# Optimization experiments

Measured on AMD Instinct MI355X. Metric: run time of the kernel, lower is better.

## Reference

```python
import jax, jax.numpy as jnp
import numpy as np

B = 64
SIZES = [5023, 1256, 314, 79, 20]
NV = [s + 1 for s in SIZES]          # vertex counts incl. padding vertex
K = 12                               # spiral length (all levels)
LAT = 128
ENC_F = [3, 16, 32, 64, 128]
DEC_IN = [128, 64, 32, 32, 16]
DEC_OUT = [64, 32, 32, 16, 3]


def setup_inputs() -> dict:
    keys = iter(jax.random.split(jax.random.key(0), 80))

    def nrm(shape, scale=1.0):
        return jax.random.normal(next(keys), shape, jnp.float32) * scale

    inp = {}
    inp['x_talking'] = nrm((B, NV[0], 3))
    inp['template'] = nrm((B, NV[0], 3))
    for i in range(4):
        inp['D%d' % i] = nrm((NV[i + 1], NV[i]), 1.0 / np.sqrt(NV[i]))
        inp['U%d' % i] = nrm((NV[i], NV[i + 1]), 1.0 / np.sqrt(NV[i + 1]))
    for i in range(4):
        fan = ENC_F[i] * K
        inp['enc_w%d' % i] = nrm((ENC_F[i + 1], fan), 1.0 / np.sqrt(fan))
        inp['enc_b%d' % i] = jnp.zeros((ENC_F[i + 1],), jnp.float32)
    inp['fc_enc_w'] = nrm((LAT, NV[4] * DEC_IN[0]), 1.0 / np.sqrt(NV[4] * DEC_IN[0]))
    inp['fc_enc_b'] = jnp.zeros((LAT,), jnp.float32)
    inp['fc_dec_w'] = nrm((NV[4] * DEC_IN[0], 2 * LAT), 1.0 / np.sqrt(2 * LAT))
    inp['fc_dec_b'] = jnp.zeros((NV[4] * DEC_IN[0],), jnp.float32)
    for i in range(5):
        fan = DEC_IN[i] * K
        inp['dec_w%d' % i] = nrm((DEC_OUT[i], fan), 1.0 / np.sqrt(fan))
        inp['dec_b%d' % i] = jnp.zeros((DEC_OUT[i],), jnp.float32)
    for i in range(4):
        inp['S%d' % i] = jax.random.randint(next(keys), (NV[i], K), 0, NV[i], jnp.int32)
    return inp


def _spiral_conv(x, S, W, b, act):
    # x: [B, N, F]; S: [N, K] spiral neighbor indices; W: [out, K*F] (torch Linear layout)
    Bv, Nv, F = x.shape
    g = x[:, S, :].reshape(Bv, Nv, K * F)            # spiral neighbor gather
    y = act(jnp.einsum('bnf,of->bno', g, W) + b)     # gather-GEMM + activation
    mask = jnp.ones((1, Nv, 1), y.dtype).at[0, -1, 0].set(0.0)  # zero out padding vertex
    return y * mask


def _forward(x_talking, template, D, U, enc, fc_enc_w, fc_enc_b, fc_dec_w, fc_dec_b, dec, S):
    elu = jax.nn.elu
    # encode_talking
    x = x_talking
    for i in range(4):
        x = _spiral_conv(x, S[i], enc[i][0], enc[i][1], elu)
        x = jnp.einsum('mn,bnf->bmf', D[i], x)       # downsample
    z = x.reshape(B, -1) @ fc_enc_w.T + fc_enc_b     # [B, latent]
    # decode(z, z)
    h = jnp.concatenate([z, z], axis=1) @ fc_dec_w.T + fc_dec_b
    x = h.reshape(B, NV[4], DEC_IN[0])
    for i in range(3):
        x = jnp.einsum('mn,bnf->bmf', U[3 - i], x)   # upsample
        x = _spiral_conv(x, S[3 - i], dec[i][0], dec[i][1], elu)
    x = jnp.einsum('mn,bnf->bmf', U[0], x)
    x = _spiral_conv(x, S[0], dec[3][0], dec[3][1], elu)
    x = _spiral_conv(x, S[0], dec[4][0], dec[4][1], lambda v: v)  # identity activation
    return x, x + template


def reference(x_talking, template, D0, D1, D2, D3, U0, U1, U2, U3,
              enc_w0, enc_b0, enc_w1, enc_b1, enc_w2, enc_b2, enc_w3, enc_b3,
              fc_enc_w, fc_enc_b, fc_dec_w, fc_dec_b,
              dec_w0, dec_b0, dec_w1, dec_b1, dec_w2, dec_b2, dec_w3, dec_b3, dec_w4, dec_b4,
              S0, S1, S2, S3):
    return _forward(
        x_talking, template,
        [D0, D1, D2, D3], [U0, U1, U2, U3],
        [(enc_w0, enc_b0), (enc_w1, enc_b1), (enc_w2, enc_b2), (enc_w3, enc_b3)],
        fc_enc_w, fc_enc_b, fc_dec_w, fc_dec_b,
        [(dec_w0, dec_b0), (dec_w1, dec_b1), (dec_w2, dec_b2), (dec_w3, dec_b3), (dec_w4, dec_b4)],
        [S0, S1, S2, S3])
```

## Files before the change

### kernel.cpp

```cpp
#include <hip/hip_runtime.h>
#include <cstddef>


#define BATCH 64
#define SPK 12

typedef __attribute__((ext_vector_type(8))) short bf16x8;
typedef __attribute__((ext_vector_type(4))) short bf16x4;
typedef __attribute__((ext_vector_type(4))) float f32x4;

__device__ __forceinline__ unsigned short f2bf(float x) {
    union { float f; unsigned int u; } v; v.f = x;
    unsigned int r = v.u + 0x7FFF + ((v.u >> 16) & 1);
    return (unsigned short)(r >> 16);
}

__global__ __launch_bounds__(256) void prep_weights_kernel(
    const float* __restrict__ enc_w0, const float* __restrict__ enc_w1,
    const float* __restrict__ enc_w2, const float* __restrict__ enc_w3,
    const float* __restrict__ dec_w0, const float* __restrict__ dec_w1,
    const float* __restrict__ dec_w2, const float* __restrict__ dec_w3,
    const float* __restrict__ dec_w4, const float* __restrict__ dec_b4,
    float* __restrict__ WpE0, unsigned short* __restrict__ Wb_e1,
    unsigned short* __restrict__ Wb_c2, unsigned short* __restrict__ Wb_e2,
    unsigned short* __restrict__ Wb_e3, unsigned short* __restrict__ Wb_c0,
    unsigned short* __restrict__ Wb_c1, unsigned short* __restrict__ Wfs_c3,
    unsigned short* __restrict__ Wfs_c4, float* __restrict__ BpC4)
{
    int i = blockIdx.x * 256 + threadIdx.x;
    if (i < 1024) {
        int o = i >> 6, kf = i & 63, k = kf >> 2, f = kf & 3;
        WpE0[i] = (f < 3 && k < 12) ? enc_w0[o * 36 + k * 3 + f] : 0.f;
        return;
    }
    i -= 1024;
    if (i < 6144)  { Wb_e1[i] = f2bf(enc_w1[i]); return; }
    i -= 6144;
    if (i < 12288) { Wb_c2[i] = f2bf(dec_w2[i]); return; }
    i -= 12288;
    if (i < 24576) { Wb_e2[i] = f2bf(enc_w2[i]); return; }
    i -= 24576;
    if (i < 98304) { Wb_e3[i] = f2bf(enc_w3[i]); return; }
    i -= 98304;
    if (i < 98304) { Wb_c0[i] = f2bf(dec_w0[i]); return; }
    i -= 98304;
    if (i < 24576) { Wb_c1[i] = f2bf(dec_w1[i]); return; }
    i -= 24576;
    if (i < 6144) {
        int j = i & 7, lane = (i >> 3) & 63, s = i >> 9;
        int l15 = lane & 15, quad = (lane >> 4) & 3;
        Wfs_c3[i] = f2bf(dec_w3[l15 * 384 + s * 32 + quad * 8 + j]);
        return;
    }
    i -= 6144;
    if (i < 3072) {
        int j = i & 7, lane = (i >> 3) & 63, s = i >> 9;
        int l15 = lane & 15, quad = (lane >> 4) & 3;
        Wfs_c4[i] = (l15 < 3) ? f2bf(dec_w4[l15 * 192 + s * 32 + quad * 8 + j])
                              : (unsigned short)0;
        return;
    }
    i -= 3072;
    if (i < 16) BpC4[i] = (i < 3) ? dec_b4[i] : 0.f;
}
#define PREP_TOTAL (1024 + 6144 + 12288 + 24576 + 98304 + 98304 + 24576 + 6144 + 3072 + 16)

__global__ __launch_bounds__(256) void reducep_bf16_kernel(
    const float* __restrict__ P, size_t ps, unsigned short* __restrict__ out,
    int n8, int nparts)
{
    int i = blockIdx.x * 256 + threadIdx.x;
    if (i < n8) {
        size_t base = (size_t)i * 8;
        bf16x8 r;
#pragma unroll
        for (int j = 0; j < 8; ++j) {
            float v = __builtin_nontemporal_load(&P[base + j]);
            for (int p = 1; p < nparts; ++p)
                v += __builtin_nontemporal_load(&P[(size_t)p * ps + base + j]);
            r[j] = (short)f2bf(v);
        }
        *(bf16x8*)(out + base) = r;
    }
}

__global__ __launch_bounds__(256) void a_bf16_pad_kernel(
    const float* __restrict__ A, unsigned short* __restrict__ Ap,
    int M, int K, int Kp, int total)
{
    int i = blockIdx.x * 256 + threadIdx.x;
    if (i >= total) return;
    int kp8 = Kp >> 3;
    int m = i / kp8;
    int k0 = (i - m * kp8) * 8;
    bf16x8 r;
    if (m < M) {
        const float* src = A + (size_t)m * K + k0;
#pragma unroll
        for (int j = 0; j < 8; ++j) {
            float v = (k0 + j < K) ? src[j] : 0.f;
            r[j] = (short)f2bf(v);
        }
    } else {
#pragma unroll
        for (int j = 0; j < 8; ++j) r[j] = 0;
    }
    *(bf16x8*)(Ap + (size_t)m * Kp + k0) = r;
}

template<int LOGF, int OBF16>
__global__ __launch_bounds__(64, 4) void conv_cmfma_kernel(
    const unsigned short* __restrict__ x, const int* __restrict__ S,
    const unsigned short* __restrict__ Wfs, const float* __restrict__ bias,
    void* __restrict__ yv, int Nv, int elu_flag, int swz)
{
    constexpr int F     = 1 << LOGF;
    constexpr int KF    = SPK * F;
    constexpr int NS    = KF / 32;
    constexpr int RPADu = (LOGF == 5) ? 40 : 24;
    __shared__ unsigned short Gs[12 * 16 * RPADu];

    const int lane = threadIdx.x;
    const int l15  = lane & 15;
    const int quad = (lane >> 4) & 3;

    int bx = blockIdx.x, bz = blockIdx.z;
    if (swz) {
        const int gx = gridDim.x;
        const int total = gx * gridDim.z;
        int bid = bx + gx * bz;
        const int chunk = total >> 3;
        int sid = (bid & 7) * chunk + (bid >> 3);
        bx = sid % gx;
        bz = sid / gx;
    }
    const int n0 = bx * 16;
    const int b  = bz;
    const size_t xb = (size_t)b * Nv;

    int4 sv;
    {
        int g = lane >> 4; if (g > 2) g = 2;
        int n = n0 + l15; if (n >= Nv) n = 0;
        sv = *(const int4*)(S + n * SPK + g * 4);
    }

    if constexpr (LOGF == 5) {
        const int grow = lane >> 2, gchk = lane & 3;
#pragma unroll
        for (int k = 0; k < 12; ++k) {
            int sel = ((k >> 2) << 4) | grow;
            int comp = k & 3;
            int src = (comp == 0) ? __shfl(sv.x, sel)
                    : (comp == 1) ? __shfl(sv.y, sel)
                    : (comp == 2) ? __shfl(sv.z, sel)
                                  : __shfl(sv.w, sel);
            bf16x8 v = *(const bf16x8*)(x + ((xb + src) << 5) + gchk * 8);
            *(bf16x8*)&Gs[k * 16 * RPADu + grow * RPADu + gchk * 8] = v;
        }
    } else {
        const int khalf = lane >> 5, grow = (lane >> 1) & 15, gchk = lane & 1;
#pragma unroll
        for (int g = 0; g < 6; ++g) {
            int k0 = 2 * g;
            int sel0 = ((k0 >> 2) << 4) | grow;
            int sel1 = (((k0 + 1) >> 2) << 4) | grow;
            int s0 = ((k0 & 3) == 0) ? __shfl(sv.x, sel0) : __shfl(sv.z, sel0);
            int s1 = (((k0 + 1) & 3) == 1) ? __shfl(sv.y, sel1) : __shfl(sv.w, sel1);
            int src = khalf ? s1 : s0;
            int k   = k0 + khalf;
            bf16x8 v = *(const bf16x8*)(x + ((xb + src) << 4) + gchk * 8);
            *(bf16x8*)&Gs[k * 16 * RPADu + grow * RPADu + gchk * 8] = v;
        }
    }

    f32x4 acc0 = (f32x4){0.f, 0.f, 0.f, 0.f};
    f32x4 acc1 = (f32x4){0.f, 0.f, 0.f, 0.f};
#pragma unroll
    for (int s = 0; s < NS; ++s) {
        int kf = s * 32 + quad * 8;
        int k  = kf >> LOGF;
        int f  = kf & (F - 1);
        bf16x8 a = *(const bf16x8*)&Gs[k * 16 * RPADu + l15 * RPADu + f];
        bf16x8 w = *(const bf16x8*)(Wfs + (s * 64 + lane) * 8);
        if (s & 1) acc1 = __builtin_amdgcn_mfma_f32_16x16x32_bf16(a, w, acc1, 0, 0, 0);
        else       acc0 = __builtin_amdgcn_mfma_f32_16x16x32_bf16(a, w, acc0, 0, 0, 0);
    }

    float bv = bias[l15];
#pragma unroll
    for (int reg = 0; reg < 4; ++reg) {
        int nn = n0 + quad * 4 + reg;
        if (nn >= Nv) continue;
        float v = acc0[reg] + acc1[reg] + bv;
        if (elu_flag && v <= 0.f) v = expm1f(v);
        if (nn == Nv - 1) v = 0.f;
        size_t off = ((size_t)b * Nv + nn) * 16 + l15;
        if (OBF16) ((unsigned short*)yv)[off] = f2bf(v);
        else       ((float*)yv)[off] = v;
    }
}

template<int LOGF, int OBF16>
__global__ __launch_bounds__(64) void conv_wmfma_kernel(
    const unsigned short* __restrict__ x, const int* __restrict__ S,
    const unsigned short* __restrict__ Wb, const float* __restrict__ bias,
    void* __restrict__ yv, int Nv, int O, int elu_flag, int swz)
{
    constexpr int F  = 1 << LOGF;
    constexpr int KF = SPK * F;
    constexpr int NS = KF / 32;
    const int lane = threadIdx.x;
    const int l15  = lane & 15;
    const int quad = lane >> 4;

    int bx = blockIdx.x, by = blockIdx.y, bz = blockIdx.z;
    if (swz) {
        const int gx = gridDim.x, gy = gridDim.y;
        const int total = gx * gy * gridDim.z;
        int bid = bx + gx * (by + gy * bz);
        const int chunk = total >> 3;
        int sid = (bid & 7) * chunk + (bid >> 3);
        bx = sid % gx; sid /= gx;
        by = sid % gy;
        bz = sid / gy;
    }

    const int n0   = bx * 16;
    const int o    = by * 16 + l15;
    const int b    = bz;
    const size_t xb = (size_t)b * Nv;

    const int n  = n0 + l15;
    const int ng = (n < Nv) ? n : 0;
    const unsigned short* wrow = Wb + (size_t)o * KF;

    f32x4 acc0 = (f32x4){0.f, 0.f, 0.f, 0.f};
    f32x4 acc1 = (f32x4){0.f, 0.f, 0.f, 0.f};
#pragma unroll
    for (int s = 0; s < NS; ++s) {
        int kf  = s * 32 + quad * 8;
        int k   = kf >> LOGF;
        int f   = kf & (F - 1);
        int src = S[ng * SPK + k];
        bf16x8 a = *(const bf16x8*)(x + ((xb + src) << LOGF) + f);
        bf16x8 w = *(const bf16x8*)(wrow + kf);
        if (s & 1) acc1 = __builtin_amdgcn_mfma_f32_16x16x32_bf16(a, w, acc1, 0, 0, 0);
        else       acc0 = __builtin_amdgcn_mfma_f32_16x16x32_bf16(a, w, acc0, 0, 0, 0);
    }
    float bv = bias[o];
#pragma unroll
    for (int reg = 0; reg < 4; ++reg) {
        int nn = n0 + quad * 4 + reg;
        if (nn >= Nv) continue;
        float v = acc0[reg] + acc1[reg] + bv;
        if (elu_flag && v <= 0.f) v = expm1f(v);
        if (nn == Nv - 1) v = 0.f;
        size_t off = ((size_t)b * Nv + nn) * O + o;
        if (OBF16) ((unsigned short*)yv)[off] = f2bf(v);
        else       ((float*)yv)[off] = v;
    }
}

template<int LOGF>
__global__ __launch_bounds__(256) void conv_mfma32_kernel(
    const unsigned short* __restrict__ x, const int* __restrict__ S,
    const unsigned short* __restrict__ Wb, const float* __restrict__ bias,
    float* __restrict__ y, int Nv, int KF, int elu_flag)
{
    constexpr int PAD = 40;
    __shared__ unsigned short Gs[2][256 * PAD];

    const int b    = blockIdx.x;
    const int n0   = blockIdx.y * 256;
    const int tid  = threadIdx.x;
    const int lane = tid & 63;
    const int wave = tid >> 6;
    const int wm   = wave * 64;
    const int l15  = lane & 15;
    const int quad = lane >> 4;
    const size_t xb = (size_t)b * Nv;
    const int nslab = KF >> 5;

    f32x4 acc[4][2];
#pragma unroll
    for (int t = 0; t < 4; ++t)
#pragma unroll
        for (int o = 0; o < 2; ++o) acc[t][o] = (f32x4){0.f, 0.f, 0.f, 0.f};

    auto gath = [&](int k0, bf16x8* g) {
        int n = n0 + tid;
        if (n < Nv) {
#pragma unroll
            for (int j = 0; j < 4; ++j) {
                int kf  = k0 + j * 8;
                int k   = kf >> LOGF;
                int f   = kf & ((1 << LOGF) - 1);
                int src = S[n * SPK + k];
                g[j] = *(const bf16x8*)(x + ((xb + src) << LOGF) + f);
            }
        } else {
#pragma unroll
            for (int j = 0; j < 4; ++j)
#pragma unroll
                for (int e = 0; e < 8; ++e) g[j][e] = 0;
        }
    };
    auto put = [&](int buf, const bf16x8* g) {
#pragma unroll
        for (int j = 0; j < 4; ++j)
            *(bf16x8*)&Gs[buf][tid * PAD + j * 8] = g[j];
    };
    auto wfrag = [&](int k0, int o16) {
        return *(const bf16x8*)(Wb + (size_t)(o16 * 16 + l15) * KF + k0 + quad * 8);
    };

    bf16x8 gcur[4], gnext[4];
    gath(0, gcur);
    put(0, gcur);
    __syncthreads();

    for (int s = 0; s < nslab; ++s) {
        const int cur = s & 1;
        const bool more = (s + 1) < nslab;
        if (more) gath((s + 1) * 32, gnext);
        bf16x8 wf0 = wfrag(s * 32, 0);
        bf16x8 wf1 = wfrag(s * 32, 1);
#pragma unroll
        for (int t = 0; t < 4; ++t) {
            bf16x8 a = *(const bf16x8*)&Gs[cur][(wm + t * 16 + l15) * PAD + quad * 8];
            acc[t][0] = __builtin_amdgcn_mfma_f32_16x16x32_bf16(a, wf0, acc[t][0], 0, 0, 0);
            acc[t][1] = __builtin_amdgcn_mfma_f32_16x16x32_bf16(a, wf1, acc[t][1], 0, 0, 0);
        }
        if (more) {
            put(cur ^ 1, gnext);
            __syncthreads();
        }
    }

    float bv0 = bias[l15];
    float bv1 = bias[16 + l15];
#pragma unroll
    for (int t = 0; t < 4; ++t)
#pragma unroll
        for (int reg = 0; reg < 4; ++reg) {
            int n = n0 + wm + t * 16 + quad * 4 + reg;
            if (n >= Nv) continue;
            float v0 = acc[t][0][reg] + bv0;
            float v1 = acc[t][1][reg] + bv1;
            if (elu_flag) {
                if (v0 <= 0.f) v0 = expm1f(v0);
                if (v1 <= 0.f) v1 = expm1f(v1);
            }
            if (n == Nv - 1) { v0 = 0.f; v1 = 0.f; }
            size_t off = ((size_t)b * Nv + n) * 32 + l15;
            y[off]      = v0;
            y[off + 16] = v1;
        }
}

template<int OBF16, int NT>
__global__ __launch_bounds__(256) void dsamp_mfma3_kernel(
    const unsigned short* __restrict__ Ab, const unsigned short* __restrict__ Xt,
    void* __restrict__ Yv, int M, int Kp, int logF, int kchunk,
    int atomic_flag, int swz, size_t pstride)
{
    constexpr int PAD = 40;
    __shared__ unsigned short As[2][128 * PAD];
    __shared__ unsigned short Bs[2][128 * PAD];

    int bx = blockIdx.x, by = blockIdx.y, bz = blockIdx.z;
    if (swz) {
        const int gx = gridDim.x, gy = gridDim.y;
        const int total = gx * gy * gridDim.z;
        int bid = bx + gx * (by + gy * bz);
        const int chunk = total >> 3;
        int sid = (bid & 7) * chunk + (bid >> 3);
        bx = sid % gx; sid /= gx;
        by = sid % gy;
        bz = sid / gy;
    }

    const int fmask = (1 << logF) - 1;
    const int m0   = bx * 128;
    const int c0   = by * 128;
    const int kbeg = bz * kchunk;
    int kend = kbeg + kchunk; if (kend > Kp) kend = Kp;
    const int nslab = (kend - kbeg + 31) >> 5;
    const size_t zoff = (size_t)bz * pstride;

    const int tid  = threadIdx.x;
    const int lane = tid & 63;
    const int wave = tid >> 6;
    const int wm   = (wave >> 1) * 64;
    const int wn   = (wave & 1) * 64;
    const int l15  = lane & 15;
    const int quad = lane >> 4;

    const int s_row = tid >> 2;
    const int s_k8  = (tid & 3) * 8;

    f32x4 acc[4][4];
#pragma unroll
    for (int i = 0; i < 4; ++i)
#pragma unroll
        for (int j = 0; j < 4; ++j) acc[i][j] = (f32x4){0.f, 0.f, 0.f, 0.f};

    bf16x8 apre[2], bpre[2];

    auto loadAB = [&](int ko) {
        apre[0] = *(const bf16x8*)(Ab + (size_t)(m0 + s_row)      * Kp + ko + s_k8);
        apre[1] = *(const bf16x8*)(Ab + (size_t)(m0 + s_row + 64) * Kp + ko + s_k8);
        bpre[0] = *(const bf16x8*)(Xt + (size_t)(c0 + s_row)      * Kp + ko + s_k8);
        bpre[1] = *(const bf16x8*)(Xt + (size_t)(c0 + s_row + 64) * Kp + ko + s_k8);
    };
    auto stage = [&](int buf) {
        *(bf16x8*)&As[buf][s_row * PAD + s_k8]        = apre[0];
        *(bf16x8*)&As[buf][(s_row + 64) * PAD + s_k8] = apre[1];
        *(bf16x8*)&Bs[buf][s_row * PAD + s_k8]        = bpre[0];
        *(bf16x8*)&Bs[buf][(s_row + 64) * PAD + s_k8] = bpre[1];
    };

    loadAB(kbeg);
    stage(0);
    __syncthreads();

    for (int s = 0; s < nslab; ++s) {
        const int cur = s & 1;
        const bool more = (s + 1) < nslab;
        if (more) loadAB(kbeg + (s + 1) * 32);

        bf16x8 af[4], bfr[4];
#pragma unroll
        for (int t = 0; t < 4; ++t) {
            af[t]  = *(const bf16x8*)&As[cur][(wm + t * 16 + l15) * PAD + quad * 8];
            bfr[t] = *(const bf16x8*)&Bs[cur][(wn + t * 16 + l15) * PAD + quad * 8];
        }
#pragma unroll
        for (int tm = 0; tm < 4; ++tm)
#pragma unroll
            for (int tn = 0; tn < 4; ++tn)
                acc[tm][tn] = __builtin_amdgcn_mfma_f32_16x16x32_bf16(af[tm], bfr[tn], acc[tm][tn], 0, 0, 0);

        if (more) { stage(cur ^ 1); __syncthreads(); }
    }

#pragma unroll
    for (int tm = 0; tm < 4; ++tm)
#pragma unroll
        for (int tn = 0; tn < 4; ++tn)
#pragma unroll
            for (int reg = 0; reg < 4; ++reg) {
                int m  = m0 + wm + tm * 16 + quad * 4 + reg;
                int cc = c0 + wn + tn * 16 + l15;
                if (m < M) {
                    int bb = cc >> logF, f = cc & fmask;
                    size_t off = zoff + (((size_t)bb * M + m) << logF) + f;
                    float v = acc[tm][tn][reg];
                    if (OBF16)            ((unsigned short*)Yv)[off] = f2bf(v);
                    else if (atomic_flag) atomicAdd((float*)Yv + off, v);
                    else if (NT)          __builtin_nontemporal_store(v, (float*)Yv + off);
                    else                  ((float*)Yv)[off] = v;
                }
            }
}

template<int OBF16, int NT>
__global__ __launch_bounds__(256) void dsamp_mfma2_kernel(
    const unsigned short* __restrict__ Ap, const float* __restrict__ X,
    void* __restrict__ Yv, int M, int K, int Kp, int logF, int kchunk,
    int atomic_flag, size_t pstride)
{
    constexpr int PAD = 40;
    __shared__ unsigned short Xs[2][64 * PAD];

    const int fmask = (1 << logF) - 1;
    const int m0   = blockIdx.x * 64;
    const int c0   = blockIdx.y * 64;
    const int kbeg = blockIdx.z * kchunk;
    int kend = kbeg + kchunk; if (kend > K) kend = K;
    const int nslab = (kend - kbeg + 31) >> 5;
    const size_t zoff = (size_t)blockIdx.z * pstride;

    const int tid  = threadIdx.x;
    const int lane = tid & 63;
    const int wave = tid >> 6;
    const int wm   = (wave >> 1) * 32;
    const int wn   = (wave & 1) * 32;
    const int l15  = lane & 15;
    const int quad = lane >> 4;

    const int skk  = tid >> 4;
    const int scg  = (tid & 15) * 4;
    const int cB   = c0 + scg;
    const int xbb  = cB >> logF;
    const int xf   = cB & fmask;
    const size_t xrowbase = (((size_t)xbb * K) << logF) + xf;

    const int mA0 = m0 + wm + l15;
    const int mA1 = mA0 + 16;
    const int kaoff = quad * 8;

    f32x4 acc[2][2];
    acc[0][0] = acc[0][1] = acc[1][0] = acc[1][1] = (f32x4){0.f, 0.f, 0.f, 0.f};

    float4 xn0, xn1;
    bf16x8 ac0, ac1, an0, an1;

    {
        int k = kbeg + skk;
        xn0 = make_float4(0.f, 0.f, 0.f, 0.f);
        if (k < kend) xn0 = *(const float4*)(X + xrowbase + ((size_t)k << logF));
        k = kbeg + 16 + skk;
        xn1 = make_float4(0.f, 0.f, 0.f, 0.f);
        if (k < kend) xn1 = *(const float4*)(X + xrowbase + ((size_t)k << logF));
        int ka = kbeg + kaoff;
        ac0 = *(const bf16x8*)(Ap + (size_t)mA0 * Kp + ka);
        ac1 = *(const bf16x8*)(Ap + (size_t)mA1 * Kp + ka);
        unsigned short* p = &Xs[0][0];
        p[(scg + 0) * PAD + skk] = f2bf(xn0.x);
        p[(scg + 1) * PAD + skk] = f2bf(xn0.y);
        p[(scg + 2) * PAD + skk] = f2bf(xn0.z);
        p[(scg + 3) * PAD + skk] = f2bf(xn0.w);
        int kk1 = 16 + skk;
        p[(scg + 0) * PAD + kk1] = f2bf(xn1.x);
        p[(scg + 1) * PAD + kk1] = f2bf(xn1.y);
        p[(scg + 2) * PAD + kk1] = f2bf(xn1.z);
        p[(scg + 3) * PAD + kk1] = f2bf(xn1.w);
    }
    __syncthreads();

    for (int s = 0; s < nslab; ++s) {
        const int cur = s & 1;
        const bool more = (s + 1 < nslab);
        if (more) {
            int k0 = kbeg + (s + 1) * 32;
            int k = k0 + skk;
            xn0 = make_float4(0.f, 0.f, 0.f, 0.f);
            if (k < kend) xn0 = *(const float4*)(X + xrowbase + ((size_t)k << logF));
            k = k0 + 16 + skk;
            xn1 = make_float4(0.f, 0.f, 0.f, 0.f);
            if (k < kend) xn1 = *(const float4*)(X + xrowbase + ((size_t)k << logF));
            int ka = k0 + kaoff;
            an0 = *(const bf16x8*)(Ap + (size_t)mA0 * Kp + ka);
            an1 = *(const bf16x8*)(Ap + (size_t)mA1 * Kp + ka);
        }
        {
            const unsigned short* p = &Xs[cur][0];
            bf16x8 b0 = *(const bf16x8*)&p[(wn +      l15) * PAD + quad * 8];
            bf16x8 b1 = *(const bf16x8*)&p[(wn + 16 + l15) * PAD + quad * 8];
            acc[0][0] = __builtin_amdgcn_mfma_f32_16x16x32_bf16(ac0, b0, acc[0][0], 0, 0, 0);
            acc[0][1] = __builtin_amdgcn_mfma_f32_16x16x32_bf16(ac0, b1, acc[0][1], 0, 0, 0);
            acc[1][0] = __builtin_amdgcn_mfma_f32_16x16x32_bf16(ac1, b0, acc[1][0], 0, 0, 0);
            acc[1][1] = __builtin_amdgcn_mfma_f32_16x16x32_bf16(ac1, b1, acc[1][1], 0, 0, 0);
        }
        if (more) {
            unsigned short* q = &Xs[cur ^ 1][0];
            q[(scg + 0) * PAD + skk] = f2bf(xn0.x);
            q[(scg + 1) * PAD + skk] = f2bf(xn0.y);
            q[(scg + 2) * PAD + skk] = f2bf(xn0.z);
            q[(scg + 3) * PAD + skk] = f2bf(xn0.w);
            int kk1 = 16 + skk;
            q[(scg + 0) * PAD + kk1] = f2bf(xn1.x);
            q[(scg + 1) * PAD + kk1] = f2bf(xn1.y);
            q[(scg + 2) * PAD + kk1] = f2bf(xn1.z);
            q[(scg + 3) * PAD + kk1] = f2bf(xn1.w);
            __syncthreads();
            ac0 = an0; ac1 = an1;
        }
    }

#pragma unroll
    for (int tm = 0; tm < 2; ++tm)
#pragma unroll
        for (int tn = 0; tn < 2; ++tn)
#pragma unroll
            for (int reg = 0; reg < 4; ++reg) {
                int m  = m0 + wm + tm * 16 + quad * 4 + reg;
                int cc = c0 + wn + tn * 16 + l15;
                if (m < M) {
                    int bb = cc >> logF, f = cc & fmask;
                    size_t off = zoff + (((size_t)bb * M + m) << logF) + f;
                    float v = acc[tm][tn][reg];
                    if (OBF16)            ((unsigned short*)Yv)[off] = f2bf(v);
                    else if (atomic_flag) atomicAdd((float*)Yv + off, v);
                    else if (NT)          __builtin_nontemporal_store(v, (float*)Yv + off);
                    else                  ((float*)Yv)[off] = v;
                }
            }
}

template<int MT, int OT>
__global__ __launch_bounds__(256) void conv_gemm_kernel(
    const float* __restrict__ x, const int* __restrict__ S,
    const float* __restrict__ W, const float* __restrict__ bias,
    float* __restrict__ y, int Nv, int logF, int O, int KF, int KFr,
    int elu_flag)
{
    constexpr int CT = OT / 4;
    constexpr int RT = 256 / CT;
    static_assert(RT * 4 == MT, "tile shape");
    __shared__ float Gs[32][MT];
    __shared__ float Ws[32][OT];

    const int b   = blockIdx.x;
    const int n0  = blockIdx.y * MT;
    const int tid = threadIdx.x;
    const int cx  = tid % CT;
    const int ry  = tid / CT;
    const int r0  = ry * 4;
    const int o0  = cx * 4;
    const int fmask = (1 << logF) - 1;
    const size_t xb = (size_t)b * Nv;

    float acc[4][4];
#pragma unroll
    for (int i = 0; i < 4; ++i)
#pragma unroll
        for (int j = 0; j < 4; ++j) acc[i][j] = 0.f;

    for (int k0 = 0; k0 < KF; k0 += 32) {
        constexpr int GSLOTS = MT * 8;
#pragma unroll
        for (int i = 0; i < GSLOTS / 256; ++i) {
            int idx = tid + i * 256;
            int r   = idx & (MT - 1);
            int jg  = idx / MT;
            int j0  = jg * 4;
            int n   = n0 + r;
            int kf  = k0 + j0;
            float4 v = make_float4(0.f, 0.f, 0.f, 0.f);
            if (n < Nv && kf < KFr) {
                int k   = kf >> logF;
                int f   = kf & fmask;
                int src = S[n * SPK + k];
                v = *(const float4*)(x + ((xb + src) << logF) + f);
            }
            Gs[j0 + 0][r] = v.x; Gs[j0 + 1][r] = v.y;
            Gs[j0 + 2][r] = v.z; Gs[j0 + 3][r] = v.w;
        }
        constexpr int WSLOTS = OT * 8;
#pragma unroll
        for (int i = 0; i < (WSLOTS + 255) / 256; ++i) {
            int idx = tid + i * 256;
            if (WSLOTS >= 256 || idx < WSLOTS) {
                int o  = idx & (OT - 1);
                int jg = idx / OT;
                int j0 = jg * 4;
                float4 v = *(const float4*)(W + (size_t)o * KF + k0 + j0);
                Ws[j0 + 0][o] = v.x; Ws[j0 + 1][o] = v.y;
                Ws[j0 + 2][o] = v.z; Ws[j0 + 3][o] = v.w;
            }
        }
        __syncthreads();
#pragma unroll
        for (int kk = 0; kk < 32; ++kk) {
            float4 g = *(const float4*)&Gs[kk][r0];
            float4 w = *(const float4*)&Ws[kk][o0];
            acc[0][0] += g.x * w.x; acc[0][1] += g.x * w.y; acc[0][2] += g.x * w.z; acc[0][3] += g.x * w.w;
            acc[1][0] += g.y * w.x; acc[1][1] += g.y * w.y; acc[1][2] += g.y * w.z; acc[1][3] += g.y * w.w;
            acc[2][0] += g.z * w.x; acc[2][1] += g.z * w.y; acc[2][2] += g.z * w.z; acc[2][3] += g.z * w.w;
            acc[3][0] += g.w * w.x; acc[3][1] += g.w * w.y; acc[3][2] += g.w * w.z; acc[3][3] += g.w * w.w;
        }
        __syncthreads();
    }

    float4 bv = *(const float4*)(bias + o0);
#pragma unroll
    for (int i = 0; i < 4; ++i) {
        int n = n0 + r0 + i;
        if (n >= Nv) continue;
        float v0 = acc[i][0] + bv.x;
        float v1 = acc[i][1] + bv.y;
        float v2 = acc[i][2] + bv.z;
        float v3 = acc[i][3] + bv.w;
        if (elu_flag) {
            v0 = v0 > 0.f ? v0 : expm1f(v0);
            v1 = v1 > 0.f ? v1 : expm1f(v1);
            v2 = v2 > 0.f ? v2 : expm1f(v2);
            v3 = v3 > 0.f ? v3 : expm1f(v3);
        }
        if (n == Nv - 1) { v0 = v1 = v2 = v3 = 0.f; }
        *(float4*)(y + ((size_t)b * Nv + n) * O + o0) = make_float4(v0, v1, v2, v3);
    }
}

template<int OBF16>
__global__ __launch_bounds__(256) void dsamp_kernel(
    const float* __restrict__ A, const float* __restrict__ X,
    void* __restrict__ Yv, int M, int N, int F)
{
    __shared__ float As[16][68];
    __shared__ float Xs[16][64];

    const int m0  = blockIdx.x * 64;
    const int c0  = blockIdx.y * 64;
    const int tid = threadIdx.x;
    const int tx  = tid & 15;
    const int ty  = tid >> 4;

    float acc[4][4];
#pragma unroll
    for (int i = 0; i < 4; ++i)
#pragma unroll
        for (int j = 0; j < 4; ++j) acc[i][j] = 0.f;

    for (int k0 = 0; k0 < N; k0 += 16) {
#pragma unroll
        for (int p = 0; p < 4; ++p) {
            int r  = (tid >> 4) + p * 16;
            int kk = tid & 15;
            int m  = m0 + r;
            int n  = k0 + kk;
            float v = 0.f;
            if (m < M && n < N) v = A[(size_t)m * N + n];
            As[kk][r] = v;
        }
        {
            int kk = tid >> 4;
            int cc = (tid & 15) * 4;
            int n  = k0 + kk;
            float4 v = make_float4(0.f, 0.f, 0.f, 0.f);
            if (n < N) {
                int c  = c0 + cc;
                int bb = c / F;
                int f  = c - bb * F;
                v = *(const float4*)(X + ((size_t)bb * N + n) * F + f);
            }
            *(float4*)&Xs[kk][cc] = v;
        }
        __syncthreads();
#pragma unroll
        for (int kk = 0; kk < 16; ++kk) {
            float4 av = *(const float4*)&As[kk][ty * 4];
            float4 xv = *(const float4*)&Xs[kk][tx * 4];
            acc[0][0] += av.x * xv.x; acc[0][1] += av.x * xv.y; acc[0][2] += av.x * xv.z; acc[0][3] += av.x * xv.w;
            acc[1][0] += av.y * xv.x; acc[1][1] += av.y * xv.y; acc[1][2] += av.y * xv.z; acc[1][3] += av.y * xv.w;
            acc[2][0] += av.z * xv.x; acc[2][1] += av.z * xv.y; acc[2][2] += av.z * xv.z; acc[2][3] += av.z * xv.w;
            acc[3][0] += av.w * xv.x; acc[3][1] += av.w * xv.y; acc[3][2] += av.w * xv.z; acc[3][3] += av.w * xv.w;
        }
        __syncthreads();
    }

    const int cbase = c0 + tx * 4;
    const int bb = cbase / F;
    const int f  = cbase - bb * F;
#pragma unroll
    for (int i = 0; i < 4; ++i) {
        int m = m0 + ty * 4 + i;
        if (m < M) {
            size_t off = ((size_t)bb * M + m) * F + f;
            if (OBF16) {
                bf16x4 v;
                v[0] = (short)f2bf(acc[i][0]); v[1] = (short)f2bf(acc[i][1]);
                v[2] = (short)f2bf(acc[i][2]); v[3] = (short)f2bf(acc[i][3]);
                *(bf16x4*)((unsigned short*)Yv + off) = v;
            } else {
                *(float4*)((float*)Yv + off) =
                    make_float4(acc[i][0], acc[i][1], acc[i][2], acc[i][3]);
            }
        }
    }
}

__global__ __launch_bounds__(256) void fc_wave_kernel(
    const float* __restrict__ in, const float* __restrict__ W,
    const float* __restrict__ bias, float* __restrict__ out,
    int In, int O, int dup)
{
    const int gw   = blockIdx.x * 4 + (threadIdx.x >> 6);
    const int lane = threadIdx.x & 63;
    const int b = gw / O;
    const int o = gw - b * O;
    const float* xr = in + (size_t)b * In;
    float acc = 0.f;
    if (dup) {
        const float* wr = W + (size_t)o * (2 * In);
        for (int k = lane; k < In; k += 64)
            acc += xr[k] * (wr[k] + wr[In + k]);
    } else {
        const float* wr = W + (size_t)o * In;
        for (int k = lane; k < In; k += 64)
            acc += xr[k] * wr[k];
    }
#pragma unroll
    for (int off = 32; off > 0; off >>= 1)
        acc += __shfl_down(acc, off, 64);
    if (lane == 0) out[(size_t)b * O + o] = acc + bias[o];
}

__global__ __launch_bounds__(256) void xpose_bf16_kernel(
    const float* __restrict__ x, unsigned short* __restrict__ xt,
    int K, int Kp, int logF)
{
    const int c  = blockIdx.y * 256 + threadIdx.x;
    const int k0 = blockIdx.x * 8;
    const int bb = c >> logF;
    const int f  = c & ((1 << logF) - 1);
    const float* src = x + (((size_t)bb * K) << logF) + f;
    bf16x8 r;
#pragma unroll
    for (int j = 0; j < 8; ++j) {
        int k = k0 + j;
        float v = (k < K) ? src[(size_t)k << logF] : 0.f;
        r[j] = (short)f2bf(v);
    }
    *(bf16x8*)(xt + (size_t)c * Kp + k0) = r;
}

__global__ __launch_bounds__(256) void pad_x4_kernel(
    const float* __restrict__ x, float* __restrict__ xp, int n)
{
    int i = blockIdx.x * 256 + threadIdx.x;
    if (i < n) {
        int f = i & 3, nb = i >> 2;
        xp[i] = (f < 3) ? x[nb * 3 + f] : 0.f;
    }
}
__global__ __launch_bounds__(256) void extract_add_kernel(
    const float* __restrict__ cp, const float* __restrict__ t,
    float* __restrict__ o0, float* __restrict__ o1, int n)
{
    int i = blockIdx.x * 256 + threadIdx.x;
    if (i < n) {
        int f = i % 3, nb = i / 3;
        float v = cp[(size_t)nb * 16 + f];
        o0[i] = v;
        o1[i] = v + t[i];
    }
}


static inline int ilog2(int v) { int l = 0; while ((1 << l) < v) ++l; return l; }

static inline void a_bf16_launch(const float* A, unsigned short* Ap, int M, int K,
                                 int Mp, int Kp, hipStream_t s)
{
    int total = Mp * (Kp >> 3);
    a_bf16_pad_kernel<<<(total + 255) / 256, 256, 0, s>>>(A, Ap, M, K, Kp, total);
}

template<int OBF16, int NT>
static inline void dsamp_mfma2_launch(const unsigned short* Ap, const float* X,
                                      void* Y, int M, int K, int Kp, int F,
                                      int ks, int partial, hipStream_t s)
{
    int kchunk = (K + ks - 1) / ks;
    kchunk = (kchunk + 31) & ~31;
    int ksz = (K + kchunk - 1) / kchunk;
    int atomic = (ksz > 1 && !partial) ? 1 : 0;
    size_t pstride = (partial && ksz > 1) ? (size_t)BATCH * M * F : 0;
    dim3 grid((M + 63) / 64, F, ksz);
    dsamp_mfma2_kernel<OBF16, NT><<<grid, 256, 0, s>>>(Ap, X, Y, M, K, Kp, ilog2(F),
                                                       kchunk, atomic, pstride);
}

template<int OBF16, int NT>
static inline void dsamp_mfma3_launch(const unsigned short* Ab, const unsigned short* Xt,
                                      void* Y, int M, int Kp, int F,
                                      int ks, int partial, hipStream_t s)
{
    int slabs = Kp >> 5;
    int kchunk = ((slabs + ks - 1) / ks) * 32;
    int ksz = (Kp + kchunk - 1) / kchunk;
    int gx = (M + 127) / 128, gy = (BATCH * F) / 128;
    int total = gx * gy * ksz;
    int swz = ((total & 7) == 0) ? 1 : 0;
    int atomic = (ksz > 1 && !partial) ? 1 : 0;
    size_t pstride = (partial && ksz > 1) ? (size_t)BATCH * M * F : 0;
    dim3 grid(gx, gy, ksz);
    dsamp_mfma3_kernel<OBF16, NT><<<grid, 256, 0, s>>>(Ab, Xt, Y, M, Kp, ilog2(F),
                                                       kchunk, atomic, swz, pstride);
}

template<int OBF16>
static inline void dsamp_launch(const float* A, const float* X, void* Y,
                                int M, int N, int F, hipStream_t s)
{
    dim3 grid((M + 63) / 64, F);
    dsamp_kernel<OBF16><<<grid, 256, 0, s>>>(A, X, Y, M, N, F);
}

extern "C" void kernel_launch(void* const* d_in, const int* in_sizes, int n_in,
                              void* d_out, int out_size, void* d_ws, size_t ws_size,
                              hipStream_t stream)
{
    const float* x_talking = (const float*)d_in[0];
    const float* templ     = (const float*)d_in[1];
    const float* D0 = (const float*)d_in[2];
    const float* U0 = (const float*)d_in[3];
    const float* D1 = (const float*)d_in[4];
    const float* U1 = (const float*)d_in[5];
    const float* D2 = (const float*)d_in[6];
    const float* U2 = (const float*)d_in[7];
    const float* D3 = (const float*)d_in[8];
    const float* U3 = (const float*)d_in[9];
    const float* enc_w0 = (const float*)d_in[10]; const float* enc_b0 = (const float*)d_in[11];
    const float* enc_w1 = (const float*)d_in[12]; const float* enc_b1 = (const float*)d_in[13];
    const float* enc_w2 = (const float*)d_in[14]; const float* enc_b2 = (const float*)d_in[15];
    const float* enc_w3 = (const float*)d_in[16]; const float* enc_b3 = (const float*)d_in[17];
    const float* fc_enc_w = (const float*)d_in[18]; const float* fc_enc_b = (const float*)d_in[19];
    const float* fc_dec_w = (const float*)d_in[20]; const float* fc_dec_b = (const float*)d_in[21];
    const float* dec_w0 = (const float*)d_in[22]; const float* dec_b0 = (const float*)d_in[23];
    const float* dec_w1 = (const float*)d_in[24]; const float* dec_b1 = (const float*)d_in[25];
    const float* dec_w2 = (const float*)d_in[26]; const float* dec_b2 = (const float*)d_in[27];
    const float* dec_w3 = (const float*)d_in[28]; const float* dec_b3 = (const float*)d_in[29];
    const float* dec_w4 = (const float*)d_in[30]; const float* dec_b4 = (const float*)d_in[31];
    const int* S0 = (const int*)d_in[32];
    const int* S1 = (const int*)d_in[33];
    const int* S2 = (const int*)d_in[34];
    const int* S3 = (const int*)d_in[35];

    float* bufA = (float*)d_ws;
    float* bufB = bufA + 10289152;

    float* out0 = (float*)d_out;
    float* out1 = out0 + 964608;

    unsigned short* Xt_e0 = (unsigned short*)(bufB + 1290240);
    unsigned short* Xt_c2 = (unsigned short*)bufB;
    unsigned short* U0b   = (unsigned short*)(bufB + 1400000);
    unsigned short* Wb_e2 = (unsigned short*)(bufB + 4700000);
    unsigned short* Wb_e3 = (unsigned short*)(bufB + 4715000);
    unsigned short* Wb_c0 = (unsigned short*)(bufB + 4765000);
    unsigned short* Wb_c1 = (unsigned short*)(bufB + 4815000);
    unsigned short* D2b   = (unsigned short*)(bufB + 4830000);
    unsigned short* U2b   = (unsigned short*)(bufB + 4860000);
    float* xpad   = bufA + 5200000;
    unsigned short* D0b   = (unsigned short*)(bufA + 6700000);
    unsigned short* D1b   = (unsigned short*)(bufA + 9950000);
    unsigned short* U1b   = (unsigned short*)(bufA + 4000000);
    unsigned short* Wb_e1 = (unsigned short*)(bufA + 10160000);
    unsigned short* Wb_c2 = (unsigned short*)(bufA + 10170000);
    unsigned short* Wfs_c3 = (unsigned short*)(bufA + 10180000);
    unsigned short* Wfs_c4 = (unsigned short*)(bufA + 10185000);
    float* BpC4   = bufA + 10190000;
    float* WpE0   = bufA + 10195000;
    float*          Pd0   = bufA;
    unsigned short* Xb_e1 = (unsigned short*)bufB;
    float*          Pd1   = bufA + 5200000;
    unsigned short* Xb_e2   = (unsigned short*)(bufA + 2000000);
    float*          Pd2   = bufB;
    unsigned short* Xb_e3   = (unsigned short*)(bufA + 2000000);
    unsigned short* Xb_c2in = (unsigned short*)(bufA + 2600000);
    unsigned short* Xb_c3n  = (unsigned short*)bufA;
    unsigned short* Xb_c4   = (unsigned short*)(bufA + 5200000);

    prep_weights_kernel<<<(PREP_TOTAL + 255) / 256, 256, 0, stream>>>(
        enc_w0, enc_w1, enc_w2, enc_w3, dec_w0, dec_w1, dec_w2, dec_w3,
        dec_w4, dec_b4, WpE0, Wb_e1, Wb_c2, Wb_e2, Wb_e3, Wb_c0, Wb_c1,
        Wfs_c3, Wfs_c4, BpC4);
    pad_x4_kernel<<<5024, 256, 0, stream>>>(x_talking, xpad, 1286144);
    a_bf16_launch(D0, D0b, 1257, 5024, 1280, 5024, stream);
    a_bf16_launch(D1, D1b, 315, 1257, 320, 1280, stream);
    a_bf16_launch(D2, D2b, 80, 315, 128, 320, stream);
    a_bf16_launch(U2, U2b, 315, 80, 320, 96, stream);

    {
        dim3 grid(BATCH, (5024 + 255) / 256);
        conv_gemm_kernel<256, 16><<<grid, 256, 0, stream>>>(
            xpad, S0, WpE0, enc_b0, bufA, 5024, 2, 16, 64, 48, 1);
    }
    xpose_bf16_kernel<<<dim3(628, 4), 256, 0, stream>>>(bufA, Xt_e0, 5024, 5024, 4);
    dsamp_mfma3_launch<0, 1>(D0b, Xt_e0, Pd0, 1257, 5024, 16, 5, 1, stream);
    reducep_bf16_kernel<<<629, 256, 0, stream>>>(Pd0, 1287168, Xb_e1, 160896, 5);
    a_bf16_launch(U0, U0b, 5024, 1257, 5120, 1280, stream);
    a_bf16_launch(U1, U1b, 1257, 315, 1280, 320, stream);
    {
        dim3 grid(BATCH, (1257 + 255) / 256);
        conv_mfma32_kernel<4><<<grid, 256, 0, stream>>>(
            Xb_e1, S1, Wb_e1, enc_b1, bufA, 1257, 192, 1);
    }
    dsamp_mfma2_launch<0, 1>(D1b, bufA, Pd1, 315, 1257, 1280, 32, 4, 1, stream);
    reducep_bf16_kernel<<<315, 256, 0, stream>>>(Pd1, 645120, Xb_e2, 80640, 4);
    {
        dim3 grid((315 + 15) / 16, 64 / 16, BATCH);
        conv_wmfma_kernel<5, 0><<<grid, 64, 0, stream>>>(
            Xb_e2, S2, Wb_e2, enc_b2, bufA, 315, 64, 1, 0);
    }
    dsamp_mfma2_launch<0, 1>(D2b, bufA, Pd2, 80, 315, 320, 64, 4, 1, stream);
    reducep_bf16_kernel<<<160, 256, 0, stream>>>(Pd2, 327680, Xb_e3, 40960, 4);
    {
        dim3 grid((80 + 15) / 16, 128 / 16, BATCH);
        conv_wmfma_kernel<6, 0><<<grid, 64, 0, stream>>>(
            Xb_e3, S3, Wb_e3, enc_b3, bufA, 80, 128, 1, 0);
    }
    dsamp_launch<0>(D3, bufA, bufB, 21, 80, 128, stream);

    fc_wave_kernel<<<dim3((BATCH * 128) / 4), 256, 0, stream>>>(bufB, fc_enc_w, fc_enc_b, bufA, 2688, 128, 0);
    fc_wave_kernel<<<dim3((BATCH * 2688) / 4), 256, 0, stream>>>(bufA, fc_dec_w, fc_dec_b, bufB, 128, 2688, 1);

    dsamp_launch<1>(U3, bufB, bufA, 80, 21, 128, stream);
    {
        dim3 grid((80 + 15) / 16, 64 / 16, BATCH);
        conv_wmfma_kernel<7, 0><<<grid, 64, 0, stream>>>(
            (const unsigned short*)bufA, S3, Wb_c0, dec_b0, bufB, 80, 64, 1, 0);
    }
    dsamp_mfma2_launch<1, 0>(U2b, bufB, bufA, 315, 80, 96, 64, 1, 0, stream);
    {
        dim3 grid((315 + 15) / 16, 32 / 16, BATCH);
        conv_wmfma_kernel<6, 0><<<grid, 64, 0, stream>>>(
            (const unsigned short*)bufA, S2, Wb_c1, dec_b1, bufB, 315, 32, 1, 0);
    }
    dsamp_mfma2_launch<1, 0>(U1b, bufB, Xb_c2in, 1257, 315, 320, 32, 1, 0, stream);
    {
        dim3 grid(BATCH, (1257 + 255) / 256);
        conv_mfma32_kernel<5><<<grid, 256, 0, stream>>>(
            Xb_c2in, S1, Wb_c2, dec_b2, bufA, 1257, 384, 1);
    }
    xpose_bf16_kernel<<<dim3(160, 8), 256, 0, stream>>>(bufA, Xt_c2, 1257, 1280, 5);
    dsamp_mfma3_launch<1, 0>(U0b, Xt_c2, Xb_c3n, 5024, 1280, 32, 1, 0, stream);

    {
        dim3 grid(5024 / 16, 1, BATCH);
        conv_cmfma_kernel<5, 1><<<grid, 64, 0, stream>>>(
            Xb_c3n, S0, Wfs_c3, dec_b3, (void*)Xb_c4, 5024, 1, 1);
    }
    {
        dim3 grid(5024 / 16, 1, BATCH);
        conv_cmfma_kernel<4, 0><<<grid, 64, 0, stream>>>(
            Xb_c4, S0, Wfs_c4, BpC4, (void*)bufB, 5024, 0, 1);
    }
    extract_add_kernel<<<(964608 + 255) / 256, 256, 0, stream>>>(bufB, templ, out0, out1, 964608);
}
```

Baseline: 648.5 us.

## Deepen global-load prefetch in the tiled bf16 MFMA GEMM to two slabs

Restructures the GEMM main loop so two K-slabs of A and B are held in registers ahead of the LDS buffer being consumed. The loop is unrolled by two, with alternating register sets and LDS buffers, so each slab's global load has more time to arrive before it is staged. Row base pointers are hoisted out of the loop. This costs extra VGPRs for the second register set, which may reduce occupancy, and adds more complex control flow for odd slab counts.

```diff
diff --git a/kernel.cpp b/kernel.cpp
--- a/kernel.cpp
+++ b/kernel.cpp
@@ -400,36 +400,38 @@
     const int s_row = tid >> 2;
     const int s_k8  = (tid & 3) * 8;
 
+    const unsigned short* pA0 = Ab + (size_t)(m0 + s_row)      * Kp + s_k8;
+    const unsigned short* pA1 = Ab + (size_t)(m0 + s_row + 64) * Kp + s_k8;
+    const unsigned short* pB0 = Xt + (size_t)(c0 + s_row)      * Kp + s_k8;
+    const unsigned short* pB1 = Xt + (size_t)(c0 + s_row + 64) * Kp + s_k8;
+
     f32x4 acc[4][4];
 #pragma unroll
     for (int i = 0; i < 4; ++i)
 #pragma unroll
         for (int j = 0; j < 4; ++j) acc[i][j] = (f32x4){0.f, 0.f, 0.f, 0.f};
 
-    bf16x8 apre[2], bpre[2];
-
-    auto loadAB = [&](int ko) {
-        apre[0] = *(const bf16x8*)(Ab + (size_t)(m0 + s_row)      * Kp + ko + s_k8);
-        apre[1] = *(const bf16x8*)(Ab + (size_t)(m0 + s_row + 64) * Kp + ko + s_k8);
-        bpre[0] = *(const bf16x8*)(Xt + (size_t)(c0 + s_row)      * Kp + ko + s_k8);
-        bpre[1] = *(const bf16x8*)(Xt + (size_t)(c0 + s_row + 64) * Kp + ko + s_k8);
-    };
-    auto stage = [&](int buf) {
-        *(bf16x8*)&As[buf][s_row * PAD + s_k8]        = apre[0];
-        *(bf16x8*)&As[buf][(s_row + 64) * PAD + s_k8] = apre[1];
-        *(bf16x8*)&Bs[buf][s_row * PAD + s_k8]        = bpre[0];
-        *(bf16x8*)&Bs[buf][(s_row + 64) * PAD + s_k8] = bpre[1];
-    };
-
-    loadAB(kbeg);
-    stage(0);
-    __syncthreads();
-
-    for (int s = 0; s < nslab; ++s) {
-        const int cur = s & 1;
-        const bool more = (s + 1) < nslab;
-        if (more) loadAB(kbeg + (s + 1) * 32);
-
+    bf16x8 ra0a, ra0b, rb0a, rb0b;
+    bf16x8 ra1a, ra1b, rb1a, rb1b;
+
+#define DS3_LOAD0(ko) do { ra0a = *(const bf16x8*)(pA0 + (ko)); \
+                           ra0b = *(const bf16x8*)(pA1 + (ko)); \
+                           rb0a = *(const bf16x8*)(pB0 + (ko)); \
+                           rb0b = *(const bf16x8*)(pB1 + (ko)); } while (0)
+#define DS3_LOAD1(ko) do { ra1a = *(const bf16x8*)(pA0 + (ko)); \
+                           ra1b = *(const bf16x8*)(pA1 + (ko)); \
+                           rb1a = *(const bf16x8*)(pB0 + (ko)); \
+                           rb1b = *(const bf16x8*)(pB1 + (ko)); } while (0)
+#define DS3_STAGE0(buf) do { *(bf16x8*)&As[buf][s_row * PAD + s_k8]        = ra0a; \
+                             *(bf16x8*)&As[buf][(s_row + 64) * PAD + s_k8] = ra0b; \
+                             *(bf16x8*)&Bs[buf][s_row * PAD + s_k8]        = rb0a; \
+                             *(bf16x8*)&Bs[buf][(s_row + 64) * PAD + s_k8] = rb0b; } while (0)
+#define DS3_STAGE1(buf) do { *(bf16x8*)&As[buf][s_row * PAD + s_k8]        = ra1a; \
+                             *(bf16x8*)&As[buf][(s_row + 64) * PAD + s_k8] = ra1b; \
+                             *(bf16x8*)&Bs[buf][s_row * PAD + s_k8]        = rb1a; \
+                             *(bf16x8*)&Bs[buf][(s_row + 64) * PAD + s_k8] = rb1b; } while (0)
+
+    auto compute = [&](int cur) {
         bf16x8 af[4], bfr[4];
 #pragma unroll
         for (int t = 0; t < 4; ++t) {
@@ -441,9 +443,35 @@
 #pragma unroll
             for (int tn = 0; tn < 4; ++tn)
                 acc[tm][tn] = __builtin_amdgcn_mfma_f32_16x16x32_bf16(af[tm], bfr[tn], acc[tm][tn], 0, 0, 0);
-
-        if (more) { stage(cur ^ 1); __syncthreads(); }
-    }
+    };
+
+    DS3_LOAD0(kbeg);
+    DS3_STAGE0(0);
+    if (nslab > 1) DS3_LOAD1(kbeg + 32);
+    if (nslab > 2) DS3_LOAD0(kbeg + 64);
+    __syncthreads();
+
+    for (int s = 0; s < nslab; s += 2) {
+        {
+            const bool more = (s + 1) < nslab;
+            if (more) DS3_STAGE1(1);
+            if (s + 3 < nslab) DS3_LOAD1(kbeg + (s + 3) * 32);
+            compute(0);
+            if (!more) break;
+            __syncthreads();
+        }
+        {
+            const bool more = (s + 2) < nslab;
+            if (more) DS3_STAGE0(0);
+            if (s + 4 < nslab) DS3_LOAD0(kbeg + (s + 4) * 32);
+            compute(1);
+            if (more) __syncthreads();
+        }
+    }
+#undef DS3_LOAD0
+#undef DS3_LOAD1
+#undef DS3_STAGE0
+#undef DS3_STAGE1
 
 #pragma unroll
     for (int tm = 0; tm < 4; ++tm)
```

Result: slower. 756.2 us (+16.6%).
